# Kernel optimization log

Hardware: AMD Instinct MI355X
Metric: run time of the kernel (lower is better)

The kernel has to match this reference:

```python
import jax, jax.numpy as jnp
import numpy as np

B = 16384      # batch
IN = 512       # input width
G, F, O = 64, 24, 16      # hidden: groups, fan_in, group_out (width = G*O = 1024)
GO_G, GO_F, GO_O = 4, 48, 16  # output layer: 4 groups x 16 = 64 outputs


def setup_inputs() -> dict:
    key = jax.random.key(0)
    ks = jax.random.split(key, 13)
    # total columns available (concat of input + all prior hidden layers)
    tot = [IN, IN + G * O, IN + 2 * G * O, IN + 3 * G * O]  # 512,1536,2560,3584
    scale = 0.1
    return {
        "x": jax.random.normal(ks[0], (B, IN), jnp.float32),
        "W1": jax.random.normal(ks[1], (G, F, O), jnp.float32) * scale,
        "b1": jnp.zeros((G, O), jnp.float32),
        "W2": jax.random.normal(ks[2], (G, F, O), jnp.float32) * scale,
        "b2": jnp.zeros((G, O), jnp.float32),
        "W3": jax.random.normal(ks[3], (G, F, O), jnp.float32) * scale,
        "b3": jnp.zeros((G, O), jnp.float32),
        "Wo": jax.random.normal(ks[4], (GO_G, GO_F, GO_O), jnp.float32) * scale,
        "bo": jnp.zeros((GO_G, GO_O), jnp.float32),
        "idx1": jax.random.randint(ks[5], (G, F), 0, tot[0], jnp.int32),
        "idx2": jax.random.randint(ks[6], (G, F), 0, tot[1], jnp.int32),
        "idx3": jax.random.randint(ks[7], (G, F), 0, tot[2], jnp.int32),
        "idxo": jax.random.randint(ks[8], (GO_G, GO_F), 0, tot[3], jnp.int32),
    }


def _group_layer(acc, idx, W, b, act):
    # acc: [B, P] concat of all prior layer outputs; idx: [G, F] column coords
    g = acc[:, idx]                               # [B, G, F] irregular gather
    h = jnp.einsum('bgf,gfo->bgo', g, W) + b      # many tiny dense sublayers
    h = act(h)
    return h.reshape(h.shape[0], -1)              # concat groups -> [B, G*O]


def reference(x, W1, b1, W2, b2, W3, b3, Wo, bo, idx1, idx2, idx3, idxo):
    acc = x
    for idx, W, b in ((idx1, W1, b1), (idx2, W2, b2), (idx3, W3, b3)):
        out = _group_layer(acc, idx, W, b, jnp.tanh)
        acc = jnp.concatenate([acc, out], axis=1)  # inputs.append(layer_out)
    # output layer uses linear out_activation
    return _group_layer(acc, idxo, Wo, bo, lambda h: h)  # [B, 64]
```

## Files before the change

### kernel.cpp

```cpp
#include <hip/hip_runtime.h>


typedef unsigned short ushort_t;
typedef unsigned int uint_t;
typedef __attribute__((ext_vector_type(8))) short short8;
typedef __attribute__((ext_vector_type(4))) float f32x4;

#define ACC_STRIDE 3592
#define ZERO_COL 3584
#define LDS_BYTES (16 * ACC_STRIDE * 2)

__device__ __forceinline__ ushort_t f2bf(float f) {
    union { float f; uint_t i; } v;
    v.f = f;
    uint_t x = v.i;
    uint_t r = (x + 0x7fffu + ((x >> 16) & 1u)) >> 16;
    return (ushort_t)r;
}

__device__ __forceinline__ uint_t pack2bf(float lo, float hi) {
    return (uint_t)f2bf(lo) | ((uint_t)f2bf(hi) << 16);
}

__device__ __forceinline__ float fast_tanh(float x) {
    float cx = fminf(fmaxf(x, -9.0f), 9.0f);
    float e = __expf(2.0f * cx);
    return (e - 1.0f) * __builtin_amdgcn_rcpf(e + 1.0f);
}

__global__ __launch_bounds__(256)
void convert_weights(const float* __restrict__ W1, const float* __restrict__ W2,
                     const float* __restrict__ W3, const float* __restrict__ Wo,
                     ushort_t* __restrict__ wfrag)
{
    const int tid = blockIdx.x * 256 + threadIdx.x;
    const int lane = tid & 63;
    const int nn = lane & 15;
    const int quad = lane >> 4;
    ushort_t v[8];
    if (tid < 12288) {
        const int g = (tid >> 6) & 63;
        const int l = tid >> 12;
        const float* W = (l == 0) ? W1 : (l == 1) ? W2 : W3;
        const float* Wg = W + g * 384;
        #pragma unroll
        for (int j = 0; j < 8; ++j) {
            const int k = quad * 8 + j;
            v[j] = (k < 24) ? f2bf(Wg[k * 16 + nn]) : (ushort_t)0;
        }
    } else if (tid < 12800) {
        const int h = tid - 12288;
        const int gs = h >> 6;
        const int go = gs >> 1;
        const int step = gs & 1;
        const float* Wg = Wo + go * 768;
        #pragma unroll
        for (int j = 0; j < 8; ++j) {
            const int k = step * 32 + quad * 8 + j;
            v[j] = (k < 48) ? f2bf(Wg[k * 16 + nn]) : (ushort_t)0;
        }
    } else {
        return;
    }
    ushort4* dst = reinterpret_cast<ushort4*>(wfrag + (size_t)tid * 8);
    dst[0] = make_ushort4(v[0], v[1], v[2], v[3]);
    dst[1] = make_ushort4(v[4], v[5], v[6], v[7]);
}

__global__ __launch_bounds__(512)
void demodel_mfma(const float* __restrict__ x,
                  const float* __restrict__ b1, const float* __restrict__ b2,
                  const float* __restrict__ b3, const float* __restrict__ bo,
                  const ushort_t* __restrict__ wfrag,
                  const int* __restrict__ idx1, const int* __restrict__ idx2,
                  const int* __restrict__ idx3, const int* __restrict__ idxo,
                  float* __restrict__ out)
{
    extern __shared__ ushort_t smem[];
    const int t = threadIdx.x;
    const int lane = t & 63;
    const int wv = t >> 6;
    const int row0 = blockIdx.x * 16;
    const int nn = lane & 15;
    const int quad = lane >> 4;
    const bool q3 = (quad == 3);

    {
        const int r = t >> 5;
        const int c = (t & 31) << 4;
        const float4* src = reinterpret_cast<const float4*>(
            x + (size_t)(row0 + r) * 512 + c);
        float4 a0 = src[0], a1 = src[1], a2 = src[2], a3 = src[3];
        uint4 p0, p1;
        p0.x = pack2bf(a0.x, a0.y); p0.y = pack2bf(a0.z, a0.w);
        p0.z = pack2bf(a1.x, a1.y); p0.w = pack2bf(a1.z, a1.w);
        p1.x = pack2bf(a2.x, a2.y); p1.y = pack2bf(a2.z, a2.w);
        p1.z = pack2bf(a3.x, a3.y); p1.w = pack2bf(a3.z, a3.w);
        uint4* dst = reinterpret_cast<uint4*>(smem + r * ACC_STRIDE + c);
        dst[0] = p0;
        dst[1] = p1;
        if (t < 16) {
            *reinterpret_cast<uint4*>(smem + t * ACC_STRIDE + ZERO_COL) =
                make_uint4(0u, 0u, 0u, 0u);
        }
    }
    __syncthreads();

    const ushort_t* acc_row = smem + nn * ACC_STRIDE;

    const int* il[3] = { idx1, idx2, idx3 };
    const float* bl[3] = { b1, b2, b3 };

    #pragma unroll 1
    for (int l = 0; l < 3; ++l) {
        const int* idxl = il[l];
        const float* bb = bl[l];
        const int out_base = 512 + l * 1024;
        #pragma unroll 1
        for (int gi = 0; gi < 8; ++gi) {
            const int g = wv * 8 + gi;
            const int ib = g * 24 + (q3 ? 0 : quad * 8);
            const int4 i0 = *reinterpret_cast<const int4*>(idxl + ib);
            const int4 i1 = *reinterpret_cast<const int4*>(idxl + ib + 4);
            short8 af;
            af[0] = (short)acc_row[q3 ? ZERO_COL : i0.x];
            af[1] = (short)acc_row[q3 ? ZERO_COL : i0.y];
            af[2] = (short)acc_row[q3 ? ZERO_COL : i0.z];
            af[3] = (short)acc_row[q3 ? ZERO_COL : i0.w];
            af[4] = (short)acc_row[q3 ? ZERO_COL : i1.x];
            af[5] = (short)acc_row[q3 ? ZERO_COL : i1.y];
            af[6] = (short)acc_row[q3 ? ZERO_COL : i1.z];
            af[7] = (short)acc_row[q3 ? ZERO_COL : i1.w];
            const short8 bf = *reinterpret_cast<const short8*>(
                wfrag + (((size_t)l * 64 + g) * 64 + lane) * 8);
            const float bv = bb[g * 16 + nn];
            f32x4 acc = { bv, bv, bv, bv };
            acc = __builtin_amdgcn_mfma_f32_16x16x32_bf16(af, bf, acc, 0, 0, 0);
            const int colo = out_base + g * 16 + nn;
            #pragma unroll
            for (int i = 0; i < 4; ++i)
                smem[(quad * 4 + i) * ACC_STRIDE + colo] = f2bf(fast_tanh(acc[i]));
        }
        __syncthreads();
    }

    if (wv < 4) {
        const int go = wv;
        const float bv = bo[go * 16 + nn];
        f32x4 acc = { bv, bv, bv, bv };
        #pragma unroll
        for (int step = 0; step < 2; ++step) {
            const int kb = step * 32 + quad * 8;
            const bool ok = (kb < 48);
            const int ib = go * 48 + (ok ? kb : 0);
            const int4 i0 = *reinterpret_cast<const int4*>(idxo + ib);
            const int4 i1 = *reinterpret_cast<const int4*>(idxo + ib + 4);
            short8 af;
            af[0] = (short)acc_row[ok ? i0.x : ZERO_COL];
            af[1] = (short)acc_row[ok ? i0.y : ZERO_COL];
            af[2] = (short)acc_row[ok ? i0.z : ZERO_COL];
            af[3] = (short)acc_row[ok ? i0.w : ZERO_COL];
            af[4] = (short)acc_row[ok ? i1.x : ZERO_COL];
            af[5] = (short)acc_row[ok ? i1.y : ZERO_COL];
            af[6] = (short)acc_row[ok ? i1.z : ZERO_COL];
            af[7] = (short)acc_row[ok ? i1.w : ZERO_COL];
            const short8 bf = *reinterpret_cast<const short8*>(
                wfrag + (12288 + ((size_t)go * 2 + step) * 64 + lane) * 8);
            acc = __builtin_amdgcn_mfma_f32_16x16x32_bf16(af, bf, acc, 0, 0, 0);
        }
        #pragma unroll
        for (int i = 0; i < 4; ++i)
            out[(size_t)(row0 + quad * 4 + i) * 64 + go * 16 + nn] = acc[i];
    }
}

extern "C" void kernel_launch(void* const* d_in, const int* in_sizes, int n_in,
                              void* d_out, int out_size, void* d_ws, size_t ws_size,
                              hipStream_t stream) {
    const float* x  = (const float*)d_in[0];
    const float* W1 = (const float*)d_in[1];
    const float* b1 = (const float*)d_in[2];
    const float* W2 = (const float*)d_in[3];
    const float* b2 = (const float*)d_in[4];
    const float* W3 = (const float*)d_in[5];
    const float* b3 = (const float*)d_in[6];
    const float* Wo = (const float*)d_in[7];
    const float* bo = (const float*)d_in[8];
    const int* idx1 = (const int*)d_in[9];
    const int* idx2 = (const int*)d_in[10];
    const int* idx3 = (const int*)d_in[11];
    const int* idxo = (const int*)d_in[12];
    float* out = (float*)d_out;

    (void)hipFuncSetAttribute((const void*)demodel_mfma,
                              hipFuncAttributeMaxDynamicSharedMemorySize,
                              LDS_BYTES);

    convert_weights<<<50, 256, 0, stream>>>(W1, W2, W3, Wo, (ushort_t*)d_ws);

    const int B = in_sizes[0] / 512;
    const int grid = B / 16;
    demodel_mfma<<<grid, 512, LDS_BYTES, stream>>>(
        x, b1, b2, b3, bo, (const ushort_t*)d_ws,
        idx1, idx2, idx3, idxo, out);
}
```

Baseline: 147.6 us.

## Precompute padded byte-offset gather tables in LDS and widen blocks to 1024 threads

The prep kernel now also turns the index arrays into padded byte-offset tables, with zero-column entries for the K padding. The main kernel copies these tables into LDS and gathers with plain byte offsets, which removes per-element quad selects and global index loads. The block grows to 1024 threads so each wave handles 4 groups per layer instead of 8, with the inner loop unrolled by 2. tanh drops its clamp and becomes a single fma with a reciprocal, and bf16 conversion uses the library intrinsic. In exchange, LDS per block grows and each block pays an extra table copy.

```diff
diff --git a/kernel.cpp b/kernel.cpp
--- a/kernel.cpp
+++ b/kernel.cpp
@@ -1,4 +1,5 @@
 #include <hip/hip_runtime.h>
+#include <hip/hip_bf16.h>
 
 
 typedef unsigned short ushort_t;
@@ -8,14 +9,19 @@
 
 #define ACC_STRIDE 3592
 #define ZERO_COL 3584
-#define LDS_BYTES (16 * ACC_STRIDE * 2)
+#define ACC_U16 (16 * ACC_STRIDE)
+#define OFFS_BYTES 25600
+#define LDS_BYTES (ACC_U16 * 2 + OFFS_BYTES)
+
+#define WF_HEAD_B 196608
+#define OFF_HID_B 204800
+#define OFF_HEAD_B 229376
 
 __device__ __forceinline__ ushort_t f2bf(float f) {
-    union { float f; uint_t i; } v;
-    v.f = f;
-    uint_t x = v.i;
-    uint_t r = (x + 0x7fffu + ((x >> 16) & 1u)) >> 16;
-    return (ushort_t)r;
+    __hip_bfloat16 h = __float2bfloat16(f);
+    union { __hip_bfloat16 h; ushort_t u; } v;
+    v.h = h;
+    return v.u;
 }
 
 __device__ __forceinline__ uint_t pack2bf(float lo, float hi) {
@@ -23,116 +29,129 @@
 }
 
 __device__ __forceinline__ float fast_tanh(float x) {
-    float cx = fminf(fmaxf(x, -9.0f), 9.0f);
-    float e = __expf(2.0f * cx);
-    return (e - 1.0f) * __builtin_amdgcn_rcpf(e + 1.0f);
+    float e = __expf(2.0f * x);
+    return fmaf(-2.0f, __builtin_amdgcn_rcpf(e + 1.0f), 1.0f);
 }
 
 __global__ __launch_bounds__(256)
 void convert_weights(const float* __restrict__ W1, const float* __restrict__ W2,
                      const float* __restrict__ W3, const float* __restrict__ Wo,
-                     ushort_t* __restrict__ wfrag)
+                     const int* __restrict__ idx1, const int* __restrict__ idx2,
+                     const int* __restrict__ idx3, const int* __restrict__ idxo,
+                     ushort_t* __restrict__ ws)
 {
     const int tid = blockIdx.x * 256 + threadIdx.x;
     const int lane = tid & 63;
     const int nn = lane & 15;
     const int quad = lane >> 4;
-    ushort_t v[8];
     if (tid < 12288) {
         const int g = (tid >> 6) & 63;
         const int l = tid >> 12;
         const float* W = (l == 0) ? W1 : (l == 1) ? W2 : W3;
         const float* Wg = W + g * 384;
+        ushort_t v[8];
         #pragma unroll
         for (int j = 0; j < 8; ++j) {
             const int k = quad * 8 + j;
             v[j] = (k < 24) ? f2bf(Wg[k * 16 + nn]) : (ushort_t)0;
         }
+        ushort4* dst = reinterpret_cast<ushort4*>(ws + (size_t)tid * 8);
+        dst[0] = make_ushort4(v[0], v[1], v[2], v[3]);
+        dst[1] = make_ushort4(v[4], v[5], v[6], v[7]);
     } else if (tid < 12800) {
         const int h = tid - 12288;
         const int gs = h >> 6;
         const int go = gs >> 1;
         const int step = gs & 1;
         const float* Wg = Wo + go * 768;
+        ushort_t v[8];
         #pragma unroll
         for (int j = 0; j < 8; ++j) {
             const int k = step * 32 + quad * 8 + j;
             v[j] = (k < 48) ? f2bf(Wg[k * 16 + nn]) : (ushort_t)0;
         }
-    } else {
-        return;
-    }
-    ushort4* dst = reinterpret_cast<ushort4*>(wfrag + (size_t)tid * 8);
-    dst[0] = make_ushort4(v[0], v[1], v[2], v[3]);
-    dst[1] = make_ushort4(v[4], v[5], v[6], v[7]);
-}
-
-__global__ __launch_bounds__(512)
+        ushort4* dst = reinterpret_cast<ushort4*>(ws + (size_t)tid * 8);
+        dst[0] = make_ushort4(v[0], v[1], v[2], v[3]);
+        dst[1] = make_ushort4(v[4], v[5], v[6], v[7]);
+    } else if (tid < 18944) {
+        const int e = tid - 12800;
+        const int l = e >> 11;
+        const int rem = e & 2047;
+        const int g = rem >> 5;
+        const int k = rem & 31;
+        const int* idx = (l == 0) ? idx1 : (l == 1) ? idx2 : idx3;
+        const int v = (k < 24) ? idx[g * 24 + k] * 2 : ZERO_COL * 2;
+        reinterpret_cast<int*>((char*)ws + OFF_HID_B)[e] = v;
+    } else if (tid < 19200) {
+        const int e = tid - 18944;
+        const int go = e >> 6;
+        const int k = e & 63;
+        const int v = (k < 48) ? idxo[go * 48 + k] * 2 : ZERO_COL * 2;
+        reinterpret_cast<int*>((char*)ws + OFF_HEAD_B)[e] = v;
+    }
+}
+
+__global__ __launch_bounds__(1024)
 void demodel_mfma(const float* __restrict__ x,
                   const float* __restrict__ b1, const float* __restrict__ b2,
                   const float* __restrict__ b3, const float* __restrict__ bo,
-                  const ushort_t* __restrict__ wfrag,
-                  const int* __restrict__ idx1, const int* __restrict__ idx2,
-                  const int* __restrict__ idx3, const int* __restrict__ idxo,
+                  const ushort_t* __restrict__ ws,
                   float* __restrict__ out)
 {
-    extern __shared__ ushort_t smem[];
+    extern __shared__ __align__(16) ushort_t smem[];
     const int t = threadIdx.x;
     const int lane = t & 63;
     const int wv = t >> 6;
     const int row0 = blockIdx.x * 16;
     const int nn = lane & 15;
     const int quad = lane >> 4;
-    const bool q3 = (quad == 3);
 
     {
-        const int r = t >> 5;
-        const int c = (t & 31) << 4;
+        const int r = t >> 6;
+        const int c = (t & 63) << 3;
         const float4* src = reinterpret_cast<const float4*>(
             x + (size_t)(row0 + r) * 512 + c);
-        float4 a0 = src[0], a1 = src[1], a2 = src[2], a3 = src[3];
-        uint4 p0, p1;
-        p0.x = pack2bf(a0.x, a0.y); p0.y = pack2bf(a0.z, a0.w);
-        p0.z = pack2bf(a1.x, a1.y); p0.w = pack2bf(a1.z, a1.w);
-        p1.x = pack2bf(a2.x, a2.y); p1.y = pack2bf(a2.z, a2.w);
-        p1.z = pack2bf(a3.x, a3.y); p1.w = pack2bf(a3.z, a3.w);
-        uint4* dst = reinterpret_cast<uint4*>(smem + r * ACC_STRIDE + c);
-        dst[0] = p0;
-        dst[1] = p1;
-        if (t < 16) {
-            *reinterpret_cast<uint4*>(smem + t * ACC_STRIDE + ZERO_COL) =
-                make_uint4(0u, 0u, 0u, 0u);
-        }
+        float4 a0 = src[0], a1 = src[1];
+        uint4 p;
+        p.x = pack2bf(a0.x, a0.y); p.y = pack2bf(a0.z, a0.w);
+        p.z = pack2bf(a1.x, a1.y); p.w = pack2bf(a1.z, a1.w);
+        *reinterpret_cast<uint4*>(smem + r * ACC_STRIDE + c) = p;
+    }
+    if (t < 16)
+        *reinterpret_cast<uint4*>(smem + t * ACC_STRIDE + ZERO_COL) =
+            make_uint4(0u, 0u, 0u, 0u);
+    {
+        const uint4* src = reinterpret_cast<const uint4*>((const char*)ws + OFF_HID_B);
+        uint4* dst = reinterpret_cast<uint4*>(smem + ACC_U16);
+        for (int i = t; i < OFFS_BYTES / 16; i += 1024)
+            dst[i] = src[i];
     }
     __syncthreads();
 
-    const ushort_t* acc_row = smem + nn * ACC_STRIDE;
-
-    const int* il[3] = { idx1, idx2, idx3 };
-    const float* bl[3] = { b1, b2, b3 };
+    const int* offs = reinterpret_cast<const int*>(smem + ACC_U16);
+    const char* accb = (const char*)smem + nn * (ACC_STRIDE * 2);
 
     #pragma unroll 1
     for (int l = 0; l < 3; ++l) {
-        const int* idxl = il[l];
-        const float* bb = bl[l];
+        const float* bb = (l == 0) ? b1 : (l == 1) ? b2 : b3;
         const int out_base = 512 + l * 1024;
-        #pragma unroll 1
-        for (int gi = 0; gi < 8; ++gi) {
-            const int g = wv * 8 + gi;
-            const int ib = g * 24 + (q3 ? 0 : quad * 8);
-            const int4 i0 = *reinterpret_cast<const int4*>(idxl + ib);
-            const int4 i1 = *reinterpret_cast<const int4*>(idxl + ib + 4);
+        #pragma unroll 2
+        for (int gi = 0; gi < 4; ++gi) {
+            const int g = (wv << 2) + gi;
+            const int* op = offs + l * 2048 + g * 32 + quad * 8;
+            const int4 o0 = *reinterpret_cast<const int4*>(op);
+            const int4 o1 = *reinterpret_cast<const int4*>(op + 4);
             short8 af;
-            af[0] = (short)acc_row[q3 ? ZERO_COL : i0.x];
-            af[1] = (short)acc_row[q3 ? ZERO_COL : i0.y];
-            af[2] = (short)acc_row[q3 ? ZERO_COL : i0.z];
-            af[3] = (short)acc_row[q3 ? ZERO_COL : i0.w];
-            af[4] = (short)acc_row[q3 ? ZERO_COL : i1.x];
-            af[5] = (short)acc_row[q3 ? ZERO_COL : i1.y];
-            af[6] = (short)acc_row[q3 ? ZERO_COL : i1.z];
-            af[7] = (short)acc_row[q3 ? ZERO_COL : i1.w];
+            af[0] = *(const short*)(accb + o0.x);
+            af[1] = *(const short*)(accb + o0.y);
+            af[2] = *(const short*)(accb + o0.z);
+            af[3] = *(const short*)(accb + o0.w);
+            af[4] = *(const short*)(accb + o1.x);
+            af[5] = *(const short*)(accb + o1.y);
+            af[6] = *(const short*)(accb + o1.z);
+            af[7] = *(const short*)(accb + o1.w);
             const short8 bf = *reinterpret_cast<const short8*>(
-                wfrag + (((size_t)l * 64 + g) * 64 + lane) * 8);
+                ws + (((size_t)l * 64 + g) * 64 + lane) * 8);
             const float bv = bb[g * 16 + nn];
             f32x4 acc = { bv, bv, bv, bv };
             acc = __builtin_amdgcn_mfma_f32_16x16x32_bf16(af, bf, acc, 0, 0, 0);
@@ -149,23 +168,21 @@
         const float bv = bo[go * 16 + nn];
         f32x4 acc = { bv, bv, bv, bv };
         #pragma unroll
-        for (int step = 0; step < 2; ++step) {
-            const int kb = step * 32 + quad * 8;
-            const bool ok = (kb < 48);
-            const int ib = go * 48 + (ok ? kb : 0);
-            const int4 i0 = *reinterpret_cast<const int4*>(idxo + ib);
-            const int4 i1 = *reinterpret_cast<const int4*>(idxo + ib + 4);
+        for (int s = 0; s < 2; ++s) {
+            const int* op = offs + 6144 + go * 64 + s * 32 + quad * 8;
+            const int4 o0 = *reinterpret_cast<const int4*>(op);
+            const int4 o1 = *reinterpret_cast<const int4*>(op + 4);
             short8 af;
-            af[0] = (short)acc_row[ok ? i0.x : ZERO_COL];
-            af[1] = (short)acc_row[ok ? i0.y : ZERO_COL];
-            af[2] = (short)acc_row[ok ? i0.z : ZERO_COL];
-            af[3] = (short)acc_row[ok ? i0.w : ZERO_COL];
-            af[4] = (short)acc_row[ok ? i1.x : ZERO_COL];
-            af[5] = (short)acc_row[ok ? i1.y : ZERO_COL];
-            af[6] = (short)acc_row[ok ? i1.z : ZERO_COL];
-            af[7] = (short)acc_row[ok ? i1.w : ZERO_COL];
+            af[0] = *(const short*)(accb + o0.x);
+            af[1] = *(const short*)(accb + o0.y);
+            af[2] = *(const short*)(accb + o0.z);
+            af[3] = *(const short*)(accb + o0.w);
+            af[4] = *(const short*)(accb + o1.x);
+            af[5] = *(const short*)(accb + o1.y);
+            af[6] = *(const short*)(accb + o1.z);
+            af[7] = *(const short*)(accb + o1.w);
             const short8 bf = *reinterpret_cast<const short8*>(
-                wfrag + (12288 + ((size_t)go * 2 + step) * 64 + lane) * 8);
+                ws + (12288 + ((size_t)go * 2 + s) * 64 + lane) * 8);
             acc = __builtin_amdgcn_mfma_f32_16x16x32_bf16(af, bf, acc, 0, 0, 0);
         }
         #pragma unroll
@@ -196,11 +213,12 @@
                               hipFuncAttributeMaxDynamicSharedMemorySize,
                               LDS_BYTES);
 
-    convert_weights<<<50, 256, 0, stream>>>(W1, W2, W3, Wo, (ushort_t*)d_ws);
+    convert_weights<<<75, 256, 0, stream>>>(W1, W2, W3, Wo,
+                                            idx1, idx2, idx3, idxo,
+                                            (ushort_t*)d_ws);
 
     const int B = in_sizes[0] / 512;
     const int grid = B / 16;
-    demodel_mfma<<<grid, 512, LDS_BYTES, stream>>>(
-        x, b1, b2, b3, bo, (const ushort_t*)d_ws,
-        idx1, idx2, idx3, idxo, out);
-}
+    demodel_mfma<<<grid, 1024, LDS_BYTES, stream>>>(
+        x, b1, b2, b3, bo, (const ushort_t*)d_ws, out);
+}
```

Result: faster. 127.1 us (-13.8%).
